# Optimization experiments

Measured on AMD Instinct MI355X. Metric: run time of the kernel, lower is better.

## Reference

```python
import jax, jax.numpy as jnp
import numpy as np

B, C, H, W = 4, 256, 64, 64
C8 = C // 8
MH, MW = 256, 256  # mask input resolution


def _conv(x, w, b, pad, dil=1):
    out = jax.lax.conv_general_dilated(
        x, w, window_strides=(1, 1),
        padding=[(pad, pad), (pad, pad)],
        rhs_dilation=(dil, dil),
        dimension_numbers=("NCHW", "OIHW", "NCHW"))
    return out + b[None, :, None, None]


def setup_inputs() -> dict:
    key = jax.random.key(0)
    ks = jax.random.split(key, 16)

    def w_init(k, shape):
        fan_in = shape[1] * shape[2] * shape[3]
        bound = 1.0 / np.sqrt(fan_in)
        return jax.random.uniform(k, shape, jnp.float32, -bound, bound)

    def b_init(k, n, fan_in):
        bound = 1.0 / np.sqrt(fan_in)
        return jax.random.uniform(k, (n,), jnp.float32, -bound, bound)

    return {
        "x": jax.random.normal(ks[0], (B, C, H, W), jnp.float32),
        "mask": jax.random.uniform(ks[1], (B, 1, MH, MW), jnp.float32),
        "w_ctx": w_init(ks[2], (C, C, 7, 7)),   "b_ctx": b_init(ks[3], C, C * 49),
        "w_wide": w_init(ks[4], (C, C, 5, 5)),  "b_wide": b_init(ks[5], C, C * 25),
        "w_comb": w_init(ks[6], (C, 2 * C, 1, 1)), "b_comb": b_init(ks[7], C, 2 * C),
        "w_q": w_init(ks[8], (C8, C, 1, 1)),    "b_q": b_init(ks[9], C8, C),
        "w_k": w_init(ks[10], (C8, C, 1, 1)),   "b_k": b_init(ks[11], C8, C),
        "w_v": w_init(ks[12], (C, C, 1, 1)),    "b_v": b_init(ks[13], C, C),
    }


def reference(x, mask, w_ctx, b_ctx, w_wide, b_wide, w_comb, b_comb,
              w_q, b_q, w_k, b_k, w_v, b_v):
    local_ctx = _conv(x, w_ctx, b_ctx, pad=3, dil=1)          # [B,C,H,W]
    wide_ctx = _conv(x, w_wide, b_wide, pad=6, dil=3)         # [B,C,H,W]
    multi = _conv(jnp.concatenate([local_ctx, wide_ctx], axis=1),
                  w_comb, b_comb, pad=0)                       # [B,C,H,W]

    b, c, h, w = multi.shape
    n = h * w
    q = _conv(multi, w_q, b_q, pad=0).reshape(b, C8, n)        # [B,C/8,N]
    k = _conv(multi, w_k, b_k, pad=0).reshape(b, C8, n)        # [B,C/8,N]
    v = _conv(multi, w_v, b_v, pad=0).reshape(b, c, n)         # [B,C,N]

    scores = jnp.einsum("bcm,bcn->bmn", q, k)                  # [B,N,N]
    attn = jax.nn.softmax(scores, axis=-1)
    out = jnp.einsum("bcn,bmn->bcm", v, attn).reshape(b, c, h, w)

    # nearest-neighbor resize of mask to (h, w), matching torch F.interpolate
    mh, mw = mask.shape[2], mask.shape[3]
    idx_h = (jnp.arange(h) * mh) // h
    idx_w = (jnp.arange(w) * mw) // w
    mask_r = mask[:, :, idx_h][:, :, :, idx_w]                 # [B,1,h,w]

    return out * (1.0 + mask_r)
```

## Files before the change

kernel.cpp:

```cpp
#include <hip/hip_runtime.h>
#include <math.h>

#define BB 4
#define CC 256
#define HH 64
#define WW 64
#define NN 4096

typedef _Float16 f16x8 __attribute__((ext_vector_type(8)));
typedef float f32x4 __attribute__((ext_vector_type(4)));

__global__ __launch_bounds__(256) void pad_kernel(
    const float* __restrict__ x, _Float16* __restrict__ xpad)
{
  int blk = blockIdx.x;
  int pr = blk % 76;
  int b  = blk / 76;
  int ci = threadIdx.x;
  int r = pr - 6;
  _Float16* dst = xpad + (((size_t)b*76 + pr)*76)*256 + ci;
  if (r < 0 || r >= HH) {
    for (int pc = 0; pc < 76; ++pc) dst[(size_t)pc*256] = (_Float16)0.f;
  } else {
    const float* src = x + ((size_t)b*CC + ci)*NN + (size_t)r*WW;
    for (int pc = 0; pc < 76; ++pc) {
      int c = pc - 6;
      float v = (c >= 0 && c < WW) ? src[c] : 0.f;
      dst[(size_t)pc*256] = (_Float16)v;
    }
  }
}

__global__ __launch_bounds__(256) void wcvt_kernel(
    const float* __restrict__ src, _Float16* __restrict__ dst, int T)
{
  int co = blockIdx.x;
  int ci = threadIdx.x;
  const float* s = src + ((size_t)co*256 + ci)*T;
  for (int t = 0; t < T; ++t)
    dst[(size_t)t*65536 + co*256 + ci] = (_Float16)s[t];
}

__global__ __launch_bounds__(256) void fcvt_kernel(
    const float* __restrict__ src, _Float16* __restrict__ dst, int n)
{
  int i = blockIdx.x * 256 + threadIdx.x;
  if (i < n) dst[i] = (_Float16)src[i];
}

template<int KS, int DIL>
__device__ __forceinline__ void conv_body(
    int blk, const _Float16* __restrict__ xpad, const _Float16* __restrict__ wb,
    const float* __restrict__ bias, _Float16* __restrict__ ctx_t, int c_off,
    char* xs)
{
  int ytile = blk & 31;
  int cot = (blk >> 5) & 1;
  int b = blk >> 6;
  int y0 = ytile * 2;
  int tid = threadIdx.x;
  int lane = tid & 63;
  int wv = tid >> 6;
  int wco = wv >> 1;
  int wsp = wv & 1;
  int l15 = lane & 15;
  int lg  = lane >> 4;

  f32x4 acc[2][4];
  #pragma unroll
  for (int m = 0; m < 2; ++m)
    #pragma unroll
    for (int n = 0; n < 4; ++n) acc[m][n] = (f32x4){0.f, 0.f, 0.f, 0.f};

  for (int kh = 0; kh < KS; ++kh) {
    int prow = 6 + y0 + (kh - KS/2) * DIL;
    const uint4* src = (const uint4*)(xpad + (((size_t)b*76 + prow)*76)*256);
    __syncthreads();
    #pragma unroll
    for (int i = 0; i < 10; ++i) {
      int ch = tid + i*512;
      if (ch < 4864) {
        uint4 v = src[ch];
        int r = ch >> 5, cq = ch & 31;
        *(uint4*)(xs + r*512 + ((cq << 4) ^ ((r & 7) << 4))) = v;
      }
    }
    __syncthreads();
    for (int kw = 0; kw < KS; ++kw) {
      int dx = (kw - KS/2) * DIL;
      int tap = kh*KS + kw;
      const _Float16* wt = wb + ((size_t)tap << 16)
                              + ((size_t)(cot*128 + wco*32 + l15) << 8) + (lg << 3);
      #pragma unroll
      for (int half = 0; half < 2; ++half) {
        f16x8 w0[4], w1[4];
        #pragma unroll
        for (int kq = 0; kq < 4; ++kq) {
          int ks = half*4 + kq;
          w0[kq] = *(const f16x8*)(wt + ks*32);
          w1[kq] = *(const f16x8*)(wt + 16*256 + ks*32);
        }
        #pragma unroll
        for (int kq = 0; kq < 4; ++kq) {
          int ks = half*4 + kq;
          #pragma unroll
          for (int nf = 0; nf < 4; ++nf) {
            int r = wsp*76 + 6 + nf*16 + l15 + dx;
            f16x8 bf = *(const f16x8*)(xs + r*512 + ((ks*64 + (lg << 4)) ^ ((r & 7) << 4)));
            acc[0][nf] = __builtin_amdgcn_mfma_f32_16x16x32_f16(w0[kq], bf, acc[0][nf], 0, 0, 0);
            acc[1][nf] = __builtin_amdgcn_mfma_f32_16x16x32_f16(w1[kq], bf, acc[1][nf], 0, 0, 0);
          }
        }
      }
    }
  }

  __syncthreads();
  _Float16* ep = (_Float16*)xs;
  #pragma unroll
  for (int m = 0; m < 2; ++m)
    #pragma unroll
    for (int i = 0; i < 4; ++i) {
      int co_l = wco*32 + m*16 + lg*4 + i;
      float bs = bias[cot*128 + co_l];
      #pragma unroll
      for (int nf = 0; nf < 4; ++nf) {
        int n_l = wsp*64 + nf*16 + l15;
        ep[n_l*136 + co_l] = (_Float16)(acc[m][nf][i] + bs);
      }
    }
  __syncthreads();
  const int cbase = c_off + cot*128;
  #pragma unroll
  for (int it = 0; it < 4; ++it) {
    int idx = tid + it*512;
    int n_l = idx >> 4, q = idx & 15;
    f16x8 val = *(const f16x8*)(ep + n_l*136 + q*8);
    *(f16x8*)(ctx_t + ((size_t)b*4096 + (size_t)y0*64 + n_l)*512 + cbase + q*8) = val;
  }
}

__global__ __launch_bounds__(512, 4) void conv_both_kernel(
    const _Float16* __restrict__ xpad,
    const _Float16* __restrict__ wb7, const _Float16* __restrict__ wb5,
    const float* __restrict__ b7, const float* __restrict__ b5,
    _Float16* __restrict__ ctx_t)
{
  __shared__ __align__(16) char xs[2*76*512];
  if (blockIdx.x < 256)
    conv_body<7, 1>(blockIdx.x, xpad, wb7, b7, ctx_t, 0, xs);
  else
    conv_body<5, 3>(blockIdx.x - 256, xpad, wb5, b5, ctx_t, 256, xs);
}

template<int K, int O, int BIASMODE>
__global__ __launch_bounds__(64) void gemm_nmajor_kernel(
    const _Float16* __restrict__ A, const _Float16* __restrict__ Wt,
    const float* __restrict__ bias0, const float* __restrict__ bias1,
    _Float16* __restrict__ outh)
{
  int nt = blockIdx.x;
  int ot = blockIdx.y;
  int lane = threadIdx.x;
  int l15 = lane & 15, lg = lane >> 4;
  int n0 = nt*64, o0 = ot*64;
  f32x4 acc[4][4] = {};
  for (int k0 = 0; k0 < K; k0 += 32) {
    f16x8 a[4], bfr[4];
    #pragma unroll
    for (int f = 0; f < 4; ++f)
      a[f] = *(const f16x8*)(A + (size_t)(n0 + f*16 + l15)*K + k0 + lg*8);
    #pragma unroll
    for (int f = 0; f < 4; ++f)
      bfr[f] = *(const f16x8*)(Wt + (size_t)(o0 + f*16 + l15)*K + k0 + lg*8);
    #pragma unroll
    for (int i = 0; i < 4; ++i)
      #pragma unroll
      for (int j = 0; j < 4; ++j)
        acc[i][j] = __builtin_amdgcn_mfma_f32_16x16x32_f16(a[i], bfr[j], acc[i][j], 0, 0, 0);
  }
  #pragma unroll
  for (int i = 0; i < 4; ++i)
    #pragma unroll
    for (int j = 0; j < 4; ++j)
      #pragma unroll
      for (int r = 0; r < 4; ++r) {
        int n = n0 + i*16 + lg*4 + r;
        int o = o0 + j*16 + l15;
        float bs = (BIASMODE == 0) ? bias0[o] : (o < 32 ? bias0[o] : bias1[o - 32]);
        outh[(size_t)n*O + o] = (_Float16)(acc[i][j][r] + bs);
      }
}

__global__ __launch_bounds__(64) void gemm_v_kernel(
    const _Float16* __restrict__ M, const _Float16* __restrict__ Wv,
    const float* __restrict__ bias, _Float16* __restrict__ v)
{
  int nt = blockIdx.x;
  int ct = blockIdx.y;
  int lane = threadIdx.x;
  int l15 = lane & 15, lg = lane >> 4;
  int n0 = nt*64, c0 = ct*64;
  f32x4 acc[4][4] = {};
  for (int k0 = 0; k0 < 256; k0 += 32) {
    f16x8 a[4], bfr[4];
    #pragma unroll
    for (int f = 0; f < 4; ++f)
      a[f] = *(const f16x8*)(Wv + (size_t)(c0 + f*16 + l15)*256 + k0 + lg*8);
    #pragma unroll
    for (int f = 0; f < 4; ++f)
      bfr[f] = *(const f16x8*)(M + (size_t)(n0 + f*16 + l15)*256 + k0 + lg*8);
    #pragma unroll
    for (int i = 0; i < 4; ++i)
      #pragma unroll
      for (int j = 0; j < 4; ++j)
        acc[i][j] = __builtin_amdgcn_mfma_f32_16x16x32_f16(a[i], bfr[j], acc[i][j], 0, 0, 0);
  }
  #pragma unroll
  for (int i = 0; i < 4; ++i)
    #pragma unroll
    for (int j = 0; j < 4; ++j)
      #pragma unroll
      for (int r = 0; r < 4; ++r) {
        int c = c0 + i*16 + lg*4 + r;
        int n_abs = n0 + j*16 + l15;
        int b = n_abs >> 12, n = n_abs & 4095;
        v[((size_t)(b*256 + c))*4096 + n] = (_Float16)(acc[i][j][r] + bias[c]);
      }
}

__global__ __launch_bounds__(256) void attn_stats_kernel(
    const _Float16* __restrict__ qh,
    float* __restrict__ rowmaxP, float* __restrict__ rowsumP)
{
  int blk = blockIdx.x;
  int b = blk >> 7, mt = (blk >> 1) & 63, nh = blk & 1;
  int tid = threadIdx.x, lane = tid & 63, w = tid >> 6;
  int l15 = lane & 15, lg = lane >> 4;
  size_t bN = (size_t)b * 4096;
  int mrow = mt*64 + w*16;
  f16x8 ah = *(const f16x8*)(qh + (bN + mrow + l15)*64 + lg*8);
  float rm[4] = {-3e38f, -3e38f, -3e38f, -3e38f};
  float sm[4] = {0.f, 0.f, 0.f, 0.f};
  for (int n0 = nh*2048; n0 < nh*2048 + 2048; n0 += 16) {
    f16x8 bh = *(const f16x8*)(qh + (bN + n0 + l15)*64 + 32 + lg*8);
    f32x4 s = {};
    s = __builtin_amdgcn_mfma_f32_16x16x32_f16(ah, bh, s, 0, 0, 0);
    #pragma unroll
    for (int i = 0; i < 4; ++i) {
      float nm = fmaxf(rm[i], s[i]);
      sm[i] = sm[i]*__expf(rm[i] - nm) + __expf(s[i] - nm);
      rm[i] = nm;
    }
  }
  #pragma unroll
  for (int off = 1; off <= 8; off <<= 1) {
    #pragma unroll
    for (int i = 0; i < 4; ++i) {
      float rmo = __shfl_xor(rm[i], off);
      float smo = __shfl_xor(sm[i], off);
      float M = fmaxf(rm[i], rmo);
      sm[i] = sm[i]*__expf(rm[i] - M) + smo*__expf(rmo - M);
      rm[i] = M;
    }
  }
  if (l15 == 0) {
    #pragma unroll
    for (int i = 0; i < 4; ++i) {
      size_t idx = (size_t)nh*16384 + bN + mrow + lg*4 + i;
      rowmaxP[idx] = rm[i];
      rowsumP[idx] = sm[i];
    }
  }
}

__global__ __launch_bounds__(512) void attn_out_kernel(
    const _Float16* __restrict__ qh, const _Float16* __restrict__ v,
    const float* __restrict__ rowmaxP, const float* __restrict__ rowsumP,
    const float* __restrict__ mask, float* __restrict__ out)
{
  __shared__ union U {
    struct { __align__(16) _Float16 vs[256*40]; __align__(16) _Float16 pl[64*40]; } s;
    float epi[256*68];
  } u;
  int blk = blockIdx.x;
  int b = blk >> 6, mt = blk & 63;
  int tid = threadIdx.x, lane = tid & 63, w = tid >> 6;
  int l15 = lane & 15, lg = lane >> 4;
  size_t bN = (size_t)b * 4096;
  int m0 = mt*64;

  int mf = w >> 1, nf2 = w & 1;
  f16x8 ah = *(const f16x8*)(qh + (bN + m0 + mf*16 + l15)*64 + lg*8);
  float rm[4], rsi[4];
  #pragma unroll
  for (int i = 0; i < 4; ++i) {
    size_t m = bN + m0 + mf*16 + lg*4 + i;
    float r0 = rowmaxP[m], r1 = rowmaxP[16384 + m];
    float s0 = rowsumP[m], s1 = rowsumP[16384 + m];
    float M = fmaxf(r0, r1);
    rm[i] = M;
    rsi[i] = 1.0f / (s0*__expf(r0 - M) + s1*__expf(r1 - M));
  }
  int mh = w >> 2, cw = (w & 3)*64;
  f32x4 acc[2][4] = {};
  const _Float16* vb = v + (size_t)b*256*4096;

  for (int n0 = 0; n0 < 4096; n0 += 32) {
    #pragma unroll
    for (int it = 0; it < 2; ++it) {
      int idx = tid + it*512;
      int c = idx >> 2, q = idx & 3;
      *(f16x8*)(u.s.vs + c*40 + q*8) = *(const f16x8*)(vb + (size_t)c*4096 + n0 + q*8);
    }
    {
      f16x8 bh = *(const f16x8*)(qh + (bN + n0 + nf2*16 + l15)*64 + 32 + lg*8);
      f32x4 s = {};
      s = __builtin_amdgcn_mfma_f32_16x16x32_f16(ah, bh, s, 0, 0, 0);
      #pragma unroll
      for (int i = 0; i < 4; ++i) {
        float p = __expf(s[i] - rm[i]) * rsi[i];
        u.s.pl[(mf*16 + lg*4 + i)*40 + nf2*16 + l15] = (_Float16)p;
      }
    }
    __syncthreads();
    {
      f16x8 pa[2], pb[4];
      #pragma unroll
      for (int af = 0; af < 2; ++af)
        pa[af] = *(const f16x8*)(u.s.pl + (mh*32 + af*16 + l15)*40 + lg*8);
      #pragma unroll
      for (int bf = 0; bf < 4; ++bf)
        pb[bf] = *(const f16x8*)(u.s.vs + (cw + bf*16 + l15)*40 + lg*8);
      #pragma unroll
      for (int af = 0; af < 2; ++af)
        #pragma unroll
        for (int bf = 0; bf < 4; ++bf)
          acc[af][bf] = __builtin_amdgcn_mfma_f32_16x16x32_f16(pa[af], pb[bf], acc[af][bf], 0, 0, 0);
    }
    __syncthreads();
  }

  #pragma unroll
  for (int af = 0; af < 2; ++af)
    #pragma unroll
    for (int bf = 0; bf < 4; ++bf)
      #pragma unroll
      for (int r = 0; r < 4; ++r) {
        int c = cw + bf*16 + l15;
        int ml = mh*32 + af*16 + lg*4 + r;
        u.epi[c*68 + ml] = acc[af][bf][r];
      }
  __syncthreads();
  const float* mb = mask + (size_t)b*65536 + (size_t)(mt*4)*256;
  #pragma unroll
  for (int it = 0; it < 8; ++it) {
    int idx = tid + it*512;
    int c = idx >> 4, q = idx & 15;
    f32x4 val = *(const f32x4*)(u.epi + c*68 + q*4);
    f32x4 o4;
    #pragma unroll
    for (int jj = 0; jj < 4; ++jj) {
      int xcol = q*4 + jj;
      o4[jj] = val[jj] * (1.0f + mb[xcol*4]);
    }
    *(f32x4*)(out + ((size_t)b*256 + c)*4096 + m0 + q*4) = o4;
  }
}

extern "C" void kernel_launch(void* const* d_in, const int* in_sizes, int n_in,
                              void* d_out, int out_size, void* d_ws, size_t ws_size,
                              hipStream_t stream)
{
  (void)in_sizes; (void)n_in; (void)out_size; (void)ws_size;
  const float* x      = (const float*)d_in[0];
  const float* mask   = (const float*)d_in[1];
  const float* w_ctx  = (const float*)d_in[2];
  const float* b_ctx  = (const float*)d_in[3];
  const float* w_wide = (const float*)d_in[4];
  const float* b_wide = (const float*)d_in[5];
  const float* w_comb = (const float*)d_in[6];
  const float* b_comb = (const float*)d_in[7];
  const float* w_q    = (const float*)d_in[8];
  const float* b_q    = (const float*)d_in[9];
  const float* w_k    = (const float*)d_in[10];
  const float* b_k    = (const float*)d_in[11];
  const float* w_v    = (const float*)d_in[12];
  const float* b_v    = (const float*)d_in[13];
  float* out = (float*)d_out;

  float* ws = (float*)d_ws;
  _Float16* xpad    = (_Float16*)(ws);
  _Float16* wb7     = (_Float16*)(ws + 2957312);
  _Float16* wb5     = (_Float16*)(ws + 4562944);
  _Float16* ctx_t   = (_Float16*)(ws + 5382144);
  _Float16* wcombH  = (_Float16*)(ws + 9576448);
  _Float16* wqkH    = (_Float16*)(ws + 9641984);
  _Float16* wvH     = (_Float16*)(ws + 9650176);
  _Float16* multi_t = (_Float16*)(ws);
  _Float16* qkt_h   = (_Float16*)(ws + 2097152);
  float*    rowmaxP = ws + 2621440;
  float*    rowsumP = ws + 2654208;
  _Float16* vbuf    = (_Float16*)(ws + 5382144);

  pad_kernel<<<BB*76, 256, 0, stream>>>(x, xpad);
  wcvt_kernel<<<256, 256, 0, stream>>>(w_ctx, wb7, 49);
  wcvt_kernel<<<256, 256, 0, stream>>>(w_wide, wb5, 25);
  fcvt_kernel<<<512, 256, 0, stream>>>(w_comb, wcombH, 131072);
  fcvt_kernel<<<32, 256, 0, stream>>>(w_q, wqkH, 8192);
  fcvt_kernel<<<32, 256, 0, stream>>>(w_k, wqkH + 8192, 8192);
  fcvt_kernel<<<256, 256, 0, stream>>>(w_v, wvH, 65536);

  conv_both_kernel<<<512, 512, 0, stream>>>(xpad, wb7, wb5, b_ctx, b_wide, ctx_t);

  gemm_nmajor_kernel<512, 256, 0><<<dim3(256, 4), 64, 0, stream>>>(
      ctx_t, wcombH, b_comb, nullptr, multi_t);
  gemm_nmajor_kernel<256, 64, 1><<<dim3(256, 1), 64, 0, stream>>>(
      multi_t, wqkH, b_q, b_k, qkt_h);
  gemm_v_kernel<<<dim3(256, 4), 64, 0, stream>>>(multi_t, wvH, b_v, vbuf);

  attn_stats_kernel<<<512, 256, 0, stream>>>(qkt_h, rowmaxP, rowsumP);
  attn_out_kernel<<<256, 512, 0, stream>>>(qkt_h, vbuf, rowmaxP, rowsumP,
                                           mask, out);
}
```

Measured before the change: 528.0 us.

## Merge prep kernels into one launch, vectorize pad loads, read V directly from global

Seven small conversion and padding kernels are merged into a single prep kernel that branches on block index, which removes per-launch overhead. The pad path now reads x as float4 and writes the border zeros in unrolled loops. Separately, attn_out_kernel stops staging V tiles in shared memory and loads the MFMA B operands straight from global memory. That shrinks LDS use and may allow higher occupancy, at the cost of less coalesced global reads repeated across waves.

```diff
diff --git a/kernel.cpp b/kernel.cpp
--- a/kernel.cpp
+++ b/kernel.cpp
@@ -10,10 +10,9 @@
 typedef _Float16 f16x8 __attribute__((ext_vector_type(8)));
 typedef float f32x4 __attribute__((ext_vector_type(4)));
 
-__global__ __launch_bounds__(256) void pad_kernel(
-    const float* __restrict__ x, _Float16* __restrict__ xpad)
-{
-  int blk = blockIdx.x;
+__device__ __forceinline__ void prep_pad(
+    int blk, const float* __restrict__ x, _Float16* __restrict__ xpad)
+{
   int pr = blk % 76;
   int b  = blk / 76;
   int ci = threadIdx.x;
@@ -22,30 +21,53 @@
   if (r < 0 || r >= HH) {
     for (int pc = 0; pc < 76; ++pc) dst[(size_t)pc*256] = (_Float16)0.f;
   } else {
-    const float* src = x + ((size_t)b*CC + ci)*NN + (size_t)r*WW;
-    for (int pc = 0; pc < 76; ++pc) {
-      int c = pc - 6;
-      float v = (c >= 0 && c < WW) ? src[c] : 0.f;
-      dst[(size_t)pc*256] = (_Float16)v;
-    }
-  }
-}
-
-__global__ __launch_bounds__(256) void wcvt_kernel(
-    const float* __restrict__ src, _Float16* __restrict__ dst, int T)
-{
-  int co = blockIdx.x;
+    #pragma unroll
+    for (int pc = 0; pc < 6; ++pc) dst[(size_t)pc*256] = (_Float16)0.f;
+    #pragma unroll
+    for (int pc = 70; pc < 76; ++pc) dst[(size_t)pc*256] = (_Float16)0.f;
+    const f32x4* s4 = (const f32x4*)(x + ((size_t)b*CC + ci)*NN + (size_t)r*WW);
+    for (int q = 0; q < 16; ++q) {
+      f32x4 v = s4[q];
+      #pragma unroll
+      for (int j = 0; j < 4; ++j)
+        dst[(size_t)(6 + q*4 + j)*256] = (_Float16)v[j];
+    }
+  }
+}
+
+__device__ __forceinline__ void prep_wcvt(
+    int co, const float* __restrict__ src, _Float16* __restrict__ dst, int T)
+{
   int ci = threadIdx.x;
   const float* s = src + ((size_t)co*256 + ci)*T;
   for (int t = 0; t < T; ++t)
     dst[(size_t)t*65536 + co*256 + ci] = (_Float16)s[t];
 }
 
-__global__ __launch_bounds__(256) void fcvt_kernel(
-    const float* __restrict__ src, _Float16* __restrict__ dst, int n)
-{
-  int i = blockIdx.x * 256 + threadIdx.x;
+__device__ __forceinline__ void prep_fcvt(
+    int blk, const float* __restrict__ src, _Float16* __restrict__ dst, int n)
+{
+  int i = blk * 256 + threadIdx.x;
   if (i < n) dst[i] = (_Float16)src[i];
+}
+
+__global__ __launch_bounds__(256) void prep_kernel(
+    const float* __restrict__ x,
+    const float* __restrict__ w_ctx, const float* __restrict__ w_wide,
+    const float* __restrict__ w_comb, const float* __restrict__ w_q,
+    const float* __restrict__ w_k, const float* __restrict__ w_v,
+    _Float16* __restrict__ xpad, _Float16* __restrict__ wb7,
+    _Float16* __restrict__ wb5, _Float16* __restrict__ wcombH,
+    _Float16* __restrict__ wqkH, _Float16* __restrict__ wvH)
+{
+  int blk = blockIdx.x;
+  if      (blk < 304)  prep_pad(blk, x, xpad);
+  else if (blk < 560)  prep_wcvt(blk - 304, w_ctx, wb7, 49);
+  else if (blk < 816)  prep_wcvt(blk - 560, w_wide, wb5, 25);
+  else if (blk < 1328) prep_fcvt(blk - 816, w_comb, wcombH, 131072);
+  else if (blk < 1360) prep_fcvt(blk - 1328, w_q, wqkH, 8192);
+  else if (blk < 1392) prep_fcvt(blk - 1360, w_k, wqkH + 8192, 8192);
+  else                 prep_fcvt(blk - 1392, w_v, wvH, 65536);
 }
 
 template<int KS, int DIL>
@@ -280,7 +302,7 @@
     const float* __restrict__ mask, float* __restrict__ out)
 {
   __shared__ union U {
-    struct { __align__(16) _Float16 vs[256*40]; __align__(16) _Float16 pl[64*40]; } s;
+    struct { __align__(16) _Float16 pl[64*40]; } s;
     float epi[256*68];
   } u;
   int blk = blockIdx.x;
@@ -307,12 +329,6 @@
   const _Float16* vb = v + (size_t)b*256*4096;
 
   for (int n0 = 0; n0 < 4096; n0 += 32) {
-    #pragma unroll
-    for (int it = 0; it < 2; ++it) {
-      int idx = tid + it*512;
-      int c = idx >> 2, q = idx & 3;
-      *(f16x8*)(u.s.vs + c*40 + q*8) = *(const f16x8*)(vb + (size_t)c*4096 + n0 + q*8);
-    }
     {
       f16x8 bh = *(const f16x8*)(qh + (bN + n0 + nf2*16 + l15)*64 + 32 + lg*8);
       f32x4 s = {};
@@ -331,7 +347,7 @@
         pa[af] = *(const f16x8*)(u.s.pl + (mh*32 + af*16 + l15)*40 + lg*8);
       #pragma unroll
       for (int bf = 0; bf < 4; ++bf)
-        pb[bf] = *(const f16x8*)(u.s.vs + (cw + bf*16 + l15)*40 + lg*8);
+        pb[bf] = *(const f16x8*)(vb + (size_t)(cw + bf*16 + l15)*4096 + n0 + lg*8);
       #pragma unroll
       for (int af = 0; af < 2; ++af)
         #pragma unroll
@@ -403,13 +419,8 @@
   float*    rowsumP = ws + 2654208;
   _Float16* vbuf    = (_Float16*)(ws + 5382144);
 
-  pad_kernel<<<BB*76, 256, 0, stream>>>(x, xpad);
-  wcvt_kernel<<<256, 256, 0, stream>>>(w_ctx, wb7, 49);
-  wcvt_kernel<<<256, 256, 0, stream>>>(w_wide, wb5, 25);
-  fcvt_kernel<<<512, 256, 0, stream>>>(w_comb, wcombH, 131072);
-  fcvt_kernel<<<32, 256, 0, stream>>>(w_q, wqkH, 8192);
-  fcvt_kernel<<<32, 256, 0, stream>>>(w_k, wqkH + 8192, 8192);
-  fcvt_kernel<<<256, 256, 0, stream>>>(w_v, wvH, 65536);
+  prep_kernel<<<1648, 256, 0, stream>>>(x, w_ctx, w_wide, w_comb, w_q, w_k,
+                                        w_v, xpad, wb7, wb5, wcombH, wqkH, wvH);
 
   conv_both_kernel<<<512, 512, 0, stream>>>(xpad, wb7, wb5, b_ctx, b_wide, ctx_t);
 
```

After: 547.1 us. +3.6%, slower.
